# Kernel optimization log

Hardware: AMD Instinct MI355X
Metric: run time of the kernel (lower is better)

Reference implementation:

```python
import jax, jax.numpy as jnp
import numpy as np


def setup_inputs() -> dict:
    key = jax.random.key(0)
    kx, kw = jax.random.split(key)
    x = jax.random.normal(kx, (32, 256, 56, 56), dtype=jnp.float32)
    # kaiming-uniform-like init for weights [O, I, K, K]
    fan_in = 256 * 3 * 3
    bound = float(np.sqrt(6.0 / fan_in))
    weights = jax.random.uniform(kw, (256, 256, 3, 3), dtype=jnp.float32,
                                 minval=-bound, maxval=bound)
    return {"x": x, "weights": weights}


def reference(x, weights):
    # Binarize weights with sign (STE is a backward-only concern; forward uses sign).
    qw = jnp.sign(weights)
    # conv2d, NCHW / OIHW, stride 1, no padding, no bias
    out = jax.lax.conv_general_dilated(
        x, qw,
        window_strides=(1, 1),
        padding="VALID",
        dimension_numbers=("NCHW", "OIHW", "NCHW"),
    )
    return out
```

## Files before the change

### kernel.cpp

```cpp
#include <hip/hip_runtime.h>
#include <cstdint>

#define NB 32
#define IC 256
#define OC 256
#define H 56
#define WIDTH 56
#define OH 54
#define OW 54
#define HW (H*WIDTH)
#define OHW (OH*OW)
#define KTOT 2304
#define M_TOT (NB*OHW)

#define BM 128
#define BO 128
#define BK 32
#define KSTEPS (KTOT/BK)
#define MBLOCKS (M_TOT/BM)

__device__ __align__(16) unsigned short g_qwt[2*KSTEPS*BO*BK];
__device__ __align__(16) unsigned short g_xq[NB*HW*IC];

typedef __bf16 bf16x8 __attribute__((ext_vector_type(8)));
typedef float  f32x4  __attribute__((ext_vector_type(4)));

typedef __attribute__((address_space(1))) const unsigned int gas_u32;
typedef __attribute__((address_space(3))) unsigned int las_u32;
__device__ __forceinline__ void async_copy16(const void* g, void* l) {
  __builtin_amdgcn_global_load_lds((gas_u32*)g, (las_u32*)l, 16, 0, 0);
}

__device__ inline unsigned short f32_bf16(float f) {
  union { float f; unsigned int u; } v; v.f = f;
  unsigned int u = v.u;
  return (unsigned short)((u + 0x7FFFu + ((u >> 16) & 1u)) >> 16);
}

__global__ __launch_bounds__(256) void repack_w(const float* __restrict__ w) {
  int L = blockIdx.x * 256 + threadIdx.x;
  int ob  = (L >= KSTEPS*BO*BK) ? 1 : 0;
  int rem = L - ob*(KSTEPS*BO*BK);
  int step = rem >> 12;
  int r    = (rem >> 5) & 127;
  int kc   = rem & 31;
  int o = ob*BO + r;
  int k = step*BK + kc;
  int pos = k >> 8;
  int c   = k & 255;
  int kh = pos / 3;
  int kw = pos - kh*3;
  float v = w[o*2304 + c*9 + kh*3 + kw];
  unsigned short s = (v > 0.f) ? 0x3F80u : ((v < 0.f) ? 0xBF80u : 0u);
  g_qwt[L] = s;
}

__global__ __launch_bounds__(256) void xform_x(const float* __restrict__ x) {
  __shared__ unsigned short tile[64][IC + 8];
  const int t   = threadIdx.x;
  const int n   = blockIdx.y;
  const int hw0 = blockIdx.x * 64;
  const int cl  = t >> 4;
  const int hl  = (t & 15) * 4;
  #pragma unroll 4
  for (int j = 0; j < 16; ++j) {
    int c = j*16 + cl;
    const float4 v = *(const float4*)(&x[(n*IC + c)*HW + hw0 + hl]);
    tile[hl+0][c] = f32_bf16(v.x);
    tile[hl+1][c] = f32_bf16(v.y);
    tile[hl+2][c] = f32_bf16(v.z);
    tile[hl+3][c] = f32_bf16(v.w);
  }
  __syncthreads();
  const int ch = (t & 31) * 8;
  const int hr = t >> 5;
  #pragma unroll
  for (int p = 0; p < 8; ++p) {
    int hwi = p*8 + hr;
    *(uint4*)(&g_xq[(n*HW + hw0 + hwi)*IC + ch]) = *(const uint4*)(&tile[hwi][ch]);
  }
}

__global__ __launch_bounds__(256) void bconv_gemm(float* __restrict__ out) {
  __shared__ __align__(16) unsigned short Wl[BO*BK];
  __shared__ __align__(16) unsigned short Xl[BM*BK];
  const int t  = threadIdx.x;
  const int m0 = blockIdx.x * BM;
  const int ob = blockIdx.y;

  int soff[2];
  #pragma unroll
  for (int hh = 0; hh < 2; ++hh) {
    int q = t + hh*256;
    int m = m0 + (q >> 2);
    int n  = m / OHW;
    int rm = m - n*OHW;
    int oh = rm / OW;
    int ow = rm - oh*OW;
    soff[hh] = ((n*H + oh)*WIDTH + ow)*IC + (q & 3)*8;
  }
  const unsigned short* wsrc = g_qwt + ob*(KSTEPS*BO*BK);

  const int lane = t & 63;
  const int wv   = t >> 6;
  const int col  = lane & 15;
  const int quad = lane >> 4;
  const int wo = (wv & 1) * 64;
  const int wm = (wv >> 1) * 64;
  int aoff[4], boff[4];
  #pragma unroll
  for (int i = 0; i < 4; ++i) {
    aoff[i] = (wo + i*16 + col)*BK + quad*8;
    boff[i] = (wm + i*16 + col)*BK + quad*8;
  }

  f32x4 acc[4][4];
  #pragma unroll
  for (int io = 0; io < 4; ++io)
    #pragma unroll
    for (int im = 0; im < 4; ++im)
      acc[io][im] = (f32x4){0.f, 0.f, 0.f, 0.f};

  for (int step = 0; step < KSTEPS; ++step) {
    const int k0  = step * BK;
    const int pos = k0 >> 8;
    const int c0  = k0 & 255;
    const int kh  = pos / 3;
    const int kw  = pos - kh*3;
    const int sk  = (kh*WIDTH + kw)*IC + c0;

    __syncthreads();
    async_copy16(&wsrc[step*(BO*BK) + t*8],         &Wl[t*8]);
    async_copy16(&wsrc[step*(BO*BK) + (t+256)*8],   &Wl[(t+256)*8]);
    async_copy16(&g_xq[soff[0] + sk],               &Xl[t*8]);
    async_copy16(&g_xq[soff[1] + sk],               &Xl[(t+256)*8]);
    __syncthreads();

    bf16x8 av[4], bv[4];
    #pragma unroll
    for (int i = 0; i < 4; ++i) av[i] = *(const bf16x8*)(&Wl[aoff[i]]);
    #pragma unroll
    for (int i = 0; i < 4; ++i) bv[i] = *(const bf16x8*)(&Xl[boff[i]]);

    #pragma unroll
    for (int io = 0; io < 4; ++io)
      #pragma unroll
      for (int im = 0; im < 4; ++im)
        acc[io][im] = __builtin_amdgcn_mfma_f32_16x16x32_bf16(av[io], bv[im], acc[io][im], 0, 0, 0);
  }

  #pragma unroll
  for (int im = 0; im < 4; ++im) {
    int m  = m0 + wm + im*16 + col;
    int n  = m / OHW;
    int rm = m - n*OHW;
    float* obase = out + n*(OC*OHW) + rm;
    #pragma unroll
    for (int io = 0; io < 4; ++io) {
      int orow = ob*BO + wo + io*16 + quad*4;
      #pragma unroll
      for (int r = 0; r < 4; ++r)
        obase[(orow + r)*OHW] = acc[io][im][r];
    }
  }
}

extern "C" void kernel_launch(void* const* d_in, const int* in_sizes, int n_in,
                              void* d_out, int out_size, void* d_ws, size_t ws_size,
                              hipStream_t stream) {
  const float* x = (const float*)d_in[0];
  const float* w = (const float*)d_in[1];
  float* out = (float*)d_out;

  repack_w<<<dim3((2*KSTEPS*BO*BK)/256), 256, 0, stream>>>(w);
  xform_x <<<dim3(HW/64, NB), 256, 0, stream>>>(x);
  bconv_gemm<<<dim3(MBLOCKS, 2), 256, 0, stream>>>(out);
}
```

Measured before the change: 359.5 us.

## Double-buffer GEMM, widen OC tile, swizzle LDS, remap XCD blocks, relayout X

The implicit-GEMM kernel now covers all 256 output channels per block with 512 threads and double-buffers the LDS tiles so the next K step's async loads overlap the current MFMAs. It also XOR-swizzles the LDS layout to cut bank conflicts and remaps block indices across XCDs for L2 locality. The input transform writes a channel-blocked (C/8, HW, 8) bf16 layout via a simpler per-thread kernel, which drops the shared-memory transpose. This costs more LDS per block and more registers, and adds hardcoded XCD arithmetic that assumes the grid size.

New measurement: 338.0 us. -6.0%, faster.

```diff
diff --git a/kernel.cpp b/kernel.cpp
--- a/kernel.cpp
+++ b/kernel.cpp
@@ -12,15 +12,16 @@
 #define OHW (OH*OW)
 #define KTOT 2304
 #define M_TOT (NB*OHW)
+#define C8N (IC/8)
 
 #define BM 128
-#define BO 128
+#define BO 256
 #define BK 32
 #define KSTEPS (KTOT/BK)
 #define MBLOCKS (M_TOT/BM)
 
-__device__ __align__(16) unsigned short g_qwt[2*KSTEPS*BO*BK];
-__device__ __align__(16) unsigned short g_xq[NB*HW*IC];
+__device__ __align__(16) unsigned short g_qwt[KSTEPS*BO*BK];
+__device__ __align__(16) unsigned short g_xq[NB*C8N*HW*8];
 
 typedef __bf16 bf16x8 __attribute__((ext_vector_type(8)));
 typedef float  f32x4  __attribute__((ext_vector_type(4)));
@@ -39,114 +40,113 @@
 
 __global__ __launch_bounds__(256) void repack_w(const float* __restrict__ w) {
   int L = blockIdx.x * 256 + threadIdx.x;
-  int ob  = (L >= KSTEPS*BO*BK) ? 1 : 0;
-  int rem = L - ob*(KSTEPS*BO*BK);
-  int step = rem >> 12;
-  int r    = (rem >> 5) & 127;
-  int kc   = rem & 31;
-  int o = ob*BO + r;
-  int k = step*BK + kc;
-  int pos = k >> 8;
-  int c   = k & 255;
-  int kh = pos / 3;
-  int kw = pos - kh*3;
-  float v = w[o*2304 + c*9 + kh*3 + kw];
+  int step = L >> 13;
+  int r    = (L >> 5) & 255;
+  int kc   = L & 31;
+  int cs   = kc >> 3;
+  int b    = kc & 7;
+  int csrc = cs ^ ((r >> 1) & 3);
+  int k    = step*BK + csrc*8 + b;
+  int pos  = k >> 8;
+  int c    = k & 255;
+  float v = w[r*2304 + c*9 + pos];
   unsigned short s = (v > 0.f) ? 0x3F80u : ((v < 0.f) ? 0xBF80u : 0u);
   g_qwt[L] = s;
 }
 
 __global__ __launch_bounds__(256) void xform_x(const float* __restrict__ x) {
-  __shared__ unsigned short tile[64][IC + 8];
-  const int t   = threadIdx.x;
-  const int n   = blockIdx.y;
-  const int hw0 = blockIdx.x * 64;
-  const int cl  = t >> 4;
-  const int hl  = (t & 15) * 4;
-  #pragma unroll 4
-  for (int j = 0; j < 16; ++j) {
-    int c = j*16 + cl;
-    const float4 v = *(const float4*)(&x[(n*IC + c)*HW + hw0 + hl]);
-    tile[hl+0][c] = f32_bf16(v.x);
-    tile[hl+1][c] = f32_bf16(v.y);
-    tile[hl+2][c] = f32_bf16(v.z);
-    tile[hl+3][c] = f32_bf16(v.w);
+  int g = blockIdx.x * 256 + threadIdx.x;
+  int hw = g % HW;
+  int tc = g / HW;
+  int c8 = tc & 31;
+  int n  = tc >> 5;
+  const float* src = x + (n*IC + c8*8)*HW + hw;
+  unsigned int o[4];
+  #pragma unroll
+  for (int j = 0; j < 4; ++j) {
+    unsigned int lo = f32_bf16(src[(2*j+0)*HW]);
+    unsigned int hi = f32_bf16(src[(2*j+1)*HW]);
+    o[j] = lo | (hi << 16);
   }
-  __syncthreads();
-  const int ch = (t & 31) * 8;
-  const int hr = t >> 5;
-  #pragma unroll
-  for (int p = 0; p < 8; ++p) {
-    int hwi = p*8 + hr;
-    *(uint4*)(&g_xq[(n*HW + hw0 + hwi)*IC + ch]) = *(const uint4*)(&tile[hwi][ch]);
-  }
+  *(uint4*)(&g_xq[g*8]) = *(uint4*)o;
 }
 
-__global__ __launch_bounds__(256) void bconv_gemm(float* __restrict__ out) {
-  __shared__ __align__(16) unsigned short Wl[BO*BK];
-  __shared__ __align__(16) unsigned short Xl[BM*BK];
-  const int t  = threadIdx.x;
-  const int m0 = blockIdx.x * BM;
-  const int ob = blockIdx.y;
+__global__ __launch_bounds__(512, 4) void bconv_gemm(float* __restrict__ out) {
+  __shared__ __align__(16) unsigned short Wl[2][BO*BK];
+  __shared__ __align__(16) unsigned short Xl[2][BM*BK];
+  const int t = threadIdx.x;
 
-  int soff[2];
-  #pragma unroll
-  for (int hh = 0; hh < 2; ++hh) {
-    int q = t + hh*256;
-    int m = m0 + (q >> 2);
+  const int orig = blockIdx.x;
+  const int xcd  = orig & 7;
+  const int idx  = orig >> 3;
+  const int bm   = (xcd == 0) ? idx : (92 + (xcd - 1)*91 + idx);
+  const int m0   = bm * BM;
+
+  int xbase;
+  {
+    const int i   = t >> 2;
+    const int cs  = t & 3;
+    const int csw = cs ^ ((i >> 1) & 3);
+    int m  = m0 + i;
     int n  = m / OHW;
     int rm = m - n*OHW;
     int oh = rm / OW;
     int ow = rm - oh*OW;
-    soff[hh] = ((n*H + oh)*WIDTH + ow)*IC + (q & 3)*8;
+    xbase = ((n*C8N + csw)*HW + oh*WIDTH + ow) * 8;
   }
-  const unsigned short* wsrc = g_qwt + ob*(KSTEPS*BO*BK);
 
   const int lane = t & 63;
   const int wv   = t >> 6;
   const int col  = lane & 15;
   const int quad = lane >> 4;
-  const int wo = (wv & 1) * 64;
-  const int wm = (wv >> 1) * 64;
+  const int wo   = (wv >> 1) * 64;
+  const int wm   = (wv & 1) * 64;
+  const int sw   = (quad ^ ((col >> 1) & 3)) * 8;
   int aoff[4], boff[4];
   #pragma unroll
   for (int i = 0; i < 4; ++i) {
-    aoff[i] = (wo + i*16 + col)*BK + quad*8;
-    boff[i] = (wm + i*16 + col)*BK + quad*8;
+    aoff[i] = (wo + i*16 + col)*BK + sw;
+    boff[i] = (wm + i*16 + col)*BK + sw;
   }
+
+  auto STAGE = [&](int step, int buf) {
+    const unsigned short* ws = g_qwt + step*(BO*BK);
+    async_copy16(&ws[t*8],       &Wl[buf][t*8]);
+    async_copy16(&ws[(t+512)*8], &Wl[buf][(t+512)*8]);
+    const int pos = step >> 3;
+    const int kh  = pos / 3;
+    const int kw  = pos - kh*3;
+    const int xo  = xbase + (((step & 7)*4)*HW + kh*WIDTH + kw)*8;
+    async_copy16(&g_xq[xo], &Xl[buf][t*8]);
+  };
 
   f32x4 acc[4][4];
   #pragma unroll
-  for (int io = 0; io < 4; ++io)
+  for (int a = 0; a < 4; ++a)
     #pragma unroll
-    for (int im = 0; im < 4; ++im)
-      acc[io][im] = (f32x4){0.f, 0.f, 0.f, 0.f};
+    for (int b = 0; b < 4; ++b)
+      acc[a][b] = (f32x4){0.f, 0.f, 0.f, 0.f};
 
+  STAGE(0, 0);
+  __syncthreads();
+  int cur = 0;
   for (int step = 0; step < KSTEPS; ++step) {
-    const int k0  = step * BK;
-    const int pos = k0 >> 8;
-    const int c0  = k0 & 255;
-    const int kh  = pos / 3;
-    const int kw  = pos - kh*3;
-    const int sk  = (kh*WIDTH + kw)*IC + c0;
-
-    __syncthreads();
-    async_copy16(&wsrc[step*(BO*BK) + t*8],         &Wl[t*8]);
-    async_copy16(&wsrc[step*(BO*BK) + (t+256)*8],   &Wl[(t+256)*8]);
-    async_copy16(&g_xq[soff[0] + sk],               &Xl[t*8]);
-    async_copy16(&g_xq[soff[1] + sk],               &Xl[(t+256)*8]);
-    __syncthreads();
+    if (step + 1 < KSTEPS) STAGE(step + 1, cur ^ 1);
 
     bf16x8 av[4], bv[4];
     #pragma unroll
-    for (int i = 0; i < 4; ++i) av[i] = *(const bf16x8*)(&Wl[aoff[i]]);
+    for (int i = 0; i < 4; ++i) av[i] = *(const bf16x8*)(&Wl[cur][aoff[i]]);
     #pragma unroll
-    for (int i = 0; i < 4; ++i) bv[i] = *(const bf16x8*)(&Xl[boff[i]]);
+    for (int i = 0; i < 4; ++i) bv[i] = *(const bf16x8*)(&Xl[cur][boff[i]]);
 
     #pragma unroll
     for (int io = 0; io < 4; ++io)
       #pragma unroll
       for (int im = 0; im < 4; ++im)
         acc[io][im] = __builtin_amdgcn_mfma_f32_16x16x32_bf16(av[io], bv[im], acc[io][im], 0, 0, 0);
+
+    __syncthreads();
+    cur ^= 1;
   }
 
   #pragma unroll
@@ -157,7 +157,7 @@
     float* obase = out + n*(OC*OHW) + rm;
     #pragma unroll
     for (int io = 0; io < 4; ++io) {
-      int orow = ob*BO + wo + io*16 + quad*4;
+      int orow = wo + io*16 + quad*4;
       #pragma unroll
       for (int r = 0; r < 4; ++r)
         obase[(orow + r)*OHW] = acc[io][im][r];
@@ -172,7 +172,7 @@
   const float* w = (const float*)d_in[1];
   float* out = (float*)d_out;
 
-  repack_w<<<dim3((2*KSTEPS*BO*BK)/256), 256, 0, stream>>>(w);
-  xform_x <<<dim3(HW/64, NB), 256, 0, stream>>>(x);
-  bconv_gemm<<<dim3(MBLOCKS, 2), 256, 0, stream>>>(out);
+  repack_w<<<dim3((KSTEPS*BO*BK)/256), 256, 0, stream>>>(w);
+  xform_x <<<dim3((NB*C8N*HW)/256), 256, 0, stream>>>(x);
+  bconv_gemm<<<dim3(MBLOCKS), 512, 0, stream>>>(out);
 }
```
